# Kernel optimization log

Measured on AMD Instinct MI355X. Metric: run time of the kernel, lower is better.

Reference implementation:

```python
import jax, jax.numpy as jnp
import numpy as np

N = 100000      # nodes
E = 3200000     # edges (avg degree 32)
F_IN = 512
F_OUT = 256


def setup_inputs() -> dict:
    key = jax.random.key(0)
    k1, k2, k3, k4, k5, k6 = jax.random.split(key, 6)
    x = jax.random.normal(k1, (N, F_IN), dtype=jnp.float32)
    row = jax.random.randint(k2, (E,), 0, N)            # destination node of each edge
    col = jax.random.randint(k3, (E,), 0, N)            # source node of each edge
    edge_val = jax.random.uniform(k4, (E,), dtype=jnp.float32)  # normalized adj weights
    stdv = 1.0 / np.sqrt(F_OUT)                         # matches reset_parameters()
    weight = jax.random.uniform(k5, (F_IN, F_OUT), dtype=jnp.float32, minval=-stdv, maxval=stdv)
    bias = jax.random.uniform(k6, (F_OUT,), dtype=jnp.float32, minval=-stdv, maxval=stdv)
    return {"input": x, "weight": weight, "bias": bias, "edge_val": edge_val, "row": row, "col": col}


def reference(input, weight, bias, edge_val, row, col):
    # support = X @ W  (dense projection)
    support = input @ weight                             # [N, F_OUT]
    # SpMM: out[r] += a[r,c] * support[c] over COO edges (torch.spmm(adj, support))
    msgs = edge_val[:, None] * support[col]              # [E, F_OUT] gather + scale
    agg = jax.ops.segment_sum(msgs, row, num_segments=input.shape[0])  # scatter-add
    # np.around(..., decimals=3) applied row-wise in the original
    out = jnp.round(agg * 1000.0) / 1000.0
    return out + bias
```

## Files before the change

### kernel.cpp

```cpp
#include <hip/hip_runtime.h>

#define N_NODES 100000
#define N_EDGES 3200000
#define FIN 512
#define FOUT 256
#define GEMM_BM 64
#define GEMM_BK 32

#define NP 782
#define CAP_LDS 4608
#define SC_CHUNK 16384

typedef __attribute__((ext_vector_type(8))) short short8;
typedef __attribute__((ext_vector_type(4))) float f32x4;

__device__ __forceinline__ unsigned short f2bf(float f) {
    unsigned u = __float_as_uint(f);
    u += 0x7fffu + ((u >> 16) & 1u);
    return (unsigned short)(u >> 16);
}
__device__ __forceinline__ float bf2f(unsigned short h) {
    return __uint_as_float(((unsigned)h) << 16);
}

__global__ __launch_bounds__(256) void prep_weight(const float* __restrict__ W,
                                                   unsigned short* __restrict__ Wt) {
    int idx = blockIdx.x * 256 + threadIdx.x;
    if (idx < FIN * FOUT) {
        int k = idx >> 8;
        int n = idx & 255;
        Wt[(size_t)(k >> 5) * (FOUT * GEMM_BK) + n * GEMM_BK + (k & 31)] = f2bf(W[idx]);
    }
}

__global__ __launch_bounds__(256, 2)
void gemm_kernel(const float* __restrict__ X, const unsigned short* __restrict__ Wt,
                 unsigned short* __restrict__ support) {
    __shared__ unsigned short A_lds[GEMM_BM][40];
    __shared__ unsigned short B_lds[FOUT][40];

    const int t = threadIdx.x;
    const int lane = t & 63;
    const int wv = t >> 6;
    const int q = lane >> 4;
    const int lr = lane & 15;
    const int m0 = blockIdx.x * GEMM_BM;

    f32x4 acc[4][4];
#pragma unroll
    for (int i = 0; i < 4; i++)
#pragma unroll
        for (int j = 0; j < 4; j++) acc[i][j] = (f32x4)0.0f;

    const int arow = t >> 2;
    const int acol = (t & 3) * 8;
    const bool avalid = (m0 + arow) < N_NODES;
    const float* Xp = X + (size_t)(m0 + arow) * FIN + acol;

    for (int s = 0; s < FIN / GEMM_BK; ++s) {
        union { unsigned short us[8]; uint4 v; } pk;
        if (avalid) {
            float4 v0 = *(const float4*)(Xp + s * GEMM_BK);
            float4 v1 = *(const float4*)(Xp + s * GEMM_BK + 4);
            pk.us[0] = f2bf(v0.x); pk.us[1] = f2bf(v0.y);
            pk.us[2] = f2bf(v0.z); pk.us[3] = f2bf(v0.w);
            pk.us[4] = f2bf(v1.x); pk.us[5] = f2bf(v1.y);
            pk.us[6] = f2bf(v1.z); pk.us[7] = f2bf(v1.w);
        } else {
            pk.v = make_uint4(0, 0, 0, 0);
        }
        const uint4* bsrc = (const uint4*)(Wt + (size_t)s * (FOUT * GEMM_BK) + t * GEMM_BK);
        uint4 b0 = bsrc[0], b1 = bsrc[1], b2 = bsrc[2], b3 = bsrc[3];

        __syncthreads();
        *(uint4*)&A_lds[arow][acol] = pk.v;
        *(uint4*)&B_lds[t][0]  = b0;
        *(uint4*)&B_lds[t][8]  = b1;
        *(uint4*)&B_lds[t][16] = b2;
        *(uint4*)&B_lds[t][24] = b3;
        __syncthreads();

        short8 af[4], bfr[4];
#pragma unroll
        for (int i = 0; i < 4; i++) af[i] = *(const short8*)&A_lds[i * 16 + lr][q * 8];
#pragma unroll
        for (int j = 0; j < 4; j++) bfr[j] = *(const short8*)&B_lds[wv * 64 + j * 16 + lr][q * 8];
#pragma unroll
        for (int i = 0; i < 4; i++)
#pragma unroll
            for (int j = 0; j < 4; j++)
                acc[i][j] = __builtin_amdgcn_mfma_f32_16x16x32_bf16(af[i], bfr[j], acc[i][j], 0, 0, 0);
    }

#pragma unroll
    for (int i = 0; i < 4; i++) {
#pragma unroll
        for (int r = 0; r < 4; r++) {
            int gm = m0 + i * 16 + q * 4 + r;
            if (gm < N_NODES) {
#pragma unroll
                for (int j = 0; j < 4; j++)
                    support[(size_t)gm * FOUT + wv * 64 + j * 16 + lr] = f2bf(acc[i][j][r]);
            }
        }
    }
}

__global__ __launch_bounds__(256) void part_hist(const int* __restrict__ row,
                                                 unsigned* __restrict__ pcnt) {
    __shared__ unsigned bins[NP];
    for (int i = threadIdx.x; i < NP; i += 256) bins[i] = 0;
    __syncthreads();
    const int e0 = blockIdx.x * 8192;
#pragma unroll
    for (int j = 0; j < 32; ++j) {
        int e = e0 + j * 256 + threadIdx.x;
        if (e < N_EDGES) atomicAdd(&bins[((unsigned)row[e]) >> 7], 1u);
    }
    __syncthreads();
    for (int i = threadIdx.x; i < NP; i += 256)
        if (bins[i]) atomicAdd(&pcnt[i], bins[i]);
}

__global__ __launch_bounds__(1024) void part_scan(const unsigned* __restrict__ pcnt,
                                                  unsigned* __restrict__ base,
                                                  unsigned* __restrict__ cursor,
                                                  unsigned* __restrict__ row_ptr) {
    __shared__ unsigned s[1024];
    const int t = threadIdx.x;
    unsigned v = (t < NP) ? pcnt[t] : 0u;
    s[t] = v;
    __syncthreads();
#pragma unroll
    for (int off = 1; off < 1024; off <<= 1) {
        unsigned tv = (t >= off) ? s[t - off] : 0u;
        __syncthreads();
        s[t] += tv;
        __syncthreads();
    }
    if (t < NP) {
        unsigned b = s[t] - v;
        base[t] = b;
        cursor[t] = b;
    }
    if (t == 0) {
        base[NP] = N_EDGES;
        row_ptr[N_NODES] = N_EDGES;
    }
}

__global__ __launch_bounds__(256) void part_scatter(const int* __restrict__ row,
                                                    const int* __restrict__ col,
                                                    const float* __restrict__ val,
                                                    unsigned* __restrict__ cursor,
                                                    uint2* __restrict__ part) {
    __shared__ unsigned bins[NP];
    __shared__ unsigned gb[NP];
    for (int i = threadIdx.x; i < NP; i += 256) bins[i] = 0;
    __syncthreads();
    const int e0 = blockIdx.x * SC_CHUNK;
#pragma unroll 4
    for (int j = 0; j < SC_CHUNK / 256; ++j) {
        int e = e0 + j * 256 + threadIdx.x;
        if (e < N_EDGES) atomicAdd(&bins[((unsigned)row[e]) >> 7], 1u);
    }
    __syncthreads();
    for (int i = threadIdx.x; i < NP; i += 256) {
        unsigned c = bins[i];
        gb[i] = c ? atomicAdd(&cursor[i], c) : 0u;
        bins[i] = 0;
    }
    __syncthreads();
#pragma unroll 4
    for (int j = 0; j < SC_CHUNK / 256; ++j) {
        int e = e0 + j * 256 + threadIdx.x;
        if (e < N_EDGES) {
            unsigned r = (unsigned)row[e];
            unsigned p = r >> 7;
            unsigned l = atomicAdd(&bins[p], 1u);
            part[gb[p] + l] = make_uint2(((unsigned)col[e]) | ((r & 127u) << 17),
                                         __float_as_uint(val[e]));
        }
    }
}

__global__ __launch_bounds__(256) void part_finalize(const unsigned* __restrict__ base,
                                                     uint2* __restrict__ part,
                                                     unsigned* __restrict__ row_ptr) {
    __shared__ uint2 recs[CAP_LDS];
    __shared__ unsigned ncnt[128], nsc[128], ccur[128];
    const int p = blockIdx.x;
    const int t = threadIdx.x;
    const unsigned b = base[p];
    unsigned cnt = base[p + 1] - b;
    if (cnt > CAP_LDS) cnt = CAP_LDS;
    if (t < 128) ncnt[t] = 0;
    __syncthreads();
    for (unsigned i = t; i < cnt; i += 256) {
        uint2 r = part[b + i];
        recs[i] = r;
        atomicAdd(&ncnt[r.x >> 17], 1u);
    }
    __syncthreads();
    if (t < 128) nsc[t] = ncnt[t];
    __syncthreads();
#pragma unroll
    for (int off = 1; off < 128; off <<= 1) {
        unsigned tv = (t < 128 && t >= off) ? nsc[t - off] : 0u;
        __syncthreads();
        if (t < 128) nsc[t] += tv;
        __syncthreads();
    }
    if (t < 128) {
        unsigned ex = nsc[t] - ncnt[t];
        ccur[t] = ex;
        int node = p * 128 + t;
        if (node < N_NODES) row_ptr[node] = b + ex;
    }
    __syncthreads();
    for (unsigned i = t; i < cnt; i += 256) {
        uint2 r = recs[i];
        unsigned pos = atomicAdd(&ccur[r.x >> 17], 1u);
        part[b + pos] = make_uint2(r.x & 0x1FFFFu, r.y);
    }
}

__global__ __launch_bounds__(256)
void spmm_kernel(const unsigned* __restrict__ row_ptr, const uint2* __restrict__ sorted,
                 const unsigned short* __restrict__ support, const float* __restrict__ bias,
                 float* __restrict__ out) {
    const int lane = threadIdx.x & 63;
    const int n = blockIdx.x * 4 + (threadIdx.x >> 6);
    const unsigned start = row_ptr[n];
    const unsigned end = row_ptr[n + 1];
    const int fo = lane * 4;
    float a0 = 0.f, a1 = 0.f, a2 = 0.f, a3 = 0.f;

    unsigned i = start;
    for (; i + 4 <= end; i += 4) {
        uint2 e0 = sorted[i], e1 = sorted[i + 1], e2 = sorted[i + 2], e3 = sorted[i + 3];
        ushort4 s0 = *(const ushort4*)(support + (size_t)e0.x * FOUT + fo);
        ushort4 s1 = *(const ushort4*)(support + (size_t)e1.x * FOUT + fo);
        ushort4 s2 = *(const ushort4*)(support + (size_t)e2.x * FOUT + fo);
        ushort4 s3 = *(const ushort4*)(support + (size_t)e3.x * FOUT + fo);
        float v0 = __uint_as_float(e0.y), v1 = __uint_as_float(e1.y);
        float v2 = __uint_as_float(e2.y), v3 = __uint_as_float(e3.y);
        a0 += v0 * bf2f(s0.x); a1 += v0 * bf2f(s0.y); a2 += v0 * bf2f(s0.z); a3 += v0 * bf2f(s0.w);
        a0 += v1 * bf2f(s1.x); a1 += v1 * bf2f(s1.y); a2 += v1 * bf2f(s1.z); a3 += v1 * bf2f(s1.w);
        a0 += v2 * bf2f(s2.x); a1 += v2 * bf2f(s2.y); a2 += v2 * bf2f(s2.z); a3 += v2 * bf2f(s2.w);
        a0 += v3 * bf2f(s3.x); a1 += v3 * bf2f(s3.y); a2 += v3 * bf2f(s3.z); a3 += v3 * bf2f(s3.w);
    }
    for (; i < end; ++i) {
        uint2 e = sorted[i];
        ushort4 s = *(const ushort4*)(support + (size_t)e.x * FOUT + fo);
        float v = __uint_as_float(e.y);
        a0 += v * bf2f(s.x); a1 += v * bf2f(s.y); a2 += v * bf2f(s.z); a3 += v * bf2f(s.w);
    }

    float4 bv = *(const float4*)(bias + fo);
    float4 r;
    r.x = rintf(a0 * 1000.f) * 0.001f + bv.x;
    r.y = rintf(a1 * 1000.f) * 0.001f + bv.y;
    r.z = rintf(a2 * 1000.f) * 0.001f + bv.z;
    r.w = rintf(a3 * 1000.f) * 0.001f + bv.w;
    *(float4*)(out + (size_t)n * FOUT + fo) = r;
}

extern "C" void kernel_launch(void* const* d_in, const int* in_sizes, int n_in,
                              void* d_out, int out_size, void* d_ws, size_t ws_size,
                              hipStream_t stream) {
    (void)in_sizes; (void)n_in; (void)out_size; (void)ws_size;
    const float* X    = (const float*)d_in[0];
    const float* W    = (const float*)d_in[1];
    const float* bias = (const float*)d_in[2];
    const float* eval = (const float*)d_in[3];
    const int*   row  = (const int*)d_in[4];
    const int*   col  = (const int*)d_in[5];
    float* out = (float*)d_out;

    char* p = (char*)d_ws;
    auto take = [&](size_t bytes) {
        char* r = p;
        p += (bytes + 511) & ~(size_t)511;
        return r;
    };
    unsigned short* support = (unsigned short*)take((size_t)N_NODES * FOUT * 2);
    unsigned short* Wt      = (unsigned short*)take((size_t)FIN * FOUT * 2);
    unsigned*       pcnt    = (unsigned*)take((size_t)NP * 4);
    unsigned*       base    = (unsigned*)take((size_t)(NP + 1) * 4);
    unsigned*       cursor  = (unsigned*)take((size_t)NP * 4);
    unsigned*       row_ptr = (unsigned*)take((size_t)(N_NODES + 1) * 4);
    uint2*          part    = (uint2*)take((size_t)N_EDGES * 8);

    hipMemsetAsync(pcnt, 0, (size_t)NP * 4, stream);
    prep_weight<<<(FIN * FOUT) / 256, 256, 0, stream>>>(W, Wt);
    gemm_kernel<<<(N_NODES + GEMM_BM - 1) / GEMM_BM, 256, 0, stream>>>(X, Wt, support);
    part_hist<<<(N_EDGES + 8191) / 8192, 256, 0, stream>>>(row, pcnt);
    part_scan<<<1, 1024, 0, stream>>>(pcnt, base, cursor, row_ptr);
    part_scatter<<<(N_EDGES + SC_CHUNK - 1) / SC_CHUNK, 256, 0, stream>>>(row, col, eval, cursor, part);
    part_finalize<<<NP, 256, 0, stream>>>(base, part, row_ptr);
    spmm_kernel<<<N_NODES / 4, 256, 0, stream>>>(row_ptr, part, support, bias, out);
}
```

Measured before the change: 738.8 us.

## Enlarge GEMM tile to 128 rows with 8 waves; pipeline SpMM edge loads

The GEMM block grows to 128 rows with 512 threads arranged as a 2x4 wave grid, so each weight tile loaded into LDS is reused across twice as many rows. fp32-to-bf16 packing now uses the HIP bf16 intrinsics. The SpMM kernel makes the row bounds wave-uniform with readfirstlane and processes edges in batches of 8, prefetching the next batch's edge records while the current batch's support rows are gathered. This raises memory-level parallelism in the gather, at the cost of more registers and lower occupancy in both kernels.

```diff
diff --git a/kernel.cpp b/kernel.cpp
--- a/kernel.cpp
+++ b/kernel.cpp
@@ -1,10 +1,11 @@
 #include <hip/hip_runtime.h>
+#include <hip/hip_bf16.h>
 
 #define N_NODES 100000
 #define N_EDGES 3200000
 #define FIN 512
 #define FOUT 256
-#define GEMM_BM 64
+#define GEMM_BM 128
 #define GEMM_BK 32
 
 #define NP 782
@@ -33,7 +34,7 @@
     }
 }
 
-__global__ __launch_bounds__(256, 2)
+__global__ __launch_bounds__(512, 4)
 void gemm_kernel(const float* __restrict__ X, const unsigned short* __restrict__ Wt,
                  unsigned short* __restrict__ support) {
     __shared__ unsigned short A_lds[GEMM_BM][40];
@@ -41,7 +42,9 @@
 
     const int t = threadIdx.x;
     const int lane = t & 63;
-    const int wv = t >> 6;
+    const int w = t >> 6;
+    const int wm = w >> 2;
+    const int wn = w & 3;
     const int q = lane >> 4;
     const int lr = lane & 15;
     const int m0 = blockIdx.x * GEMM_BM;
@@ -57,34 +60,35 @@
     const bool avalid = (m0 + arow) < N_NODES;
     const float* Xp = X + (size_t)(m0 + arow) * FIN + acol;
 
+    const int brow = t >> 1;
+    const int bcol = (t & 1) * 16;
+
     for (int s = 0; s < FIN / GEMM_BK; ++s) {
-        union { unsigned short us[8]; uint4 v; } pk;
+        union { __hip_bfloat162 h[4]; uint4 v; } pk;
         if (avalid) {
             float4 v0 = *(const float4*)(Xp + s * GEMM_BK);
             float4 v1 = *(const float4*)(Xp + s * GEMM_BK + 4);
-            pk.us[0] = f2bf(v0.x); pk.us[1] = f2bf(v0.y);
-            pk.us[2] = f2bf(v0.z); pk.us[3] = f2bf(v0.w);
-            pk.us[4] = f2bf(v1.x); pk.us[5] = f2bf(v1.y);
-            pk.us[6] = f2bf(v1.z); pk.us[7] = f2bf(v1.w);
+            pk.h[0] = __float22bfloat162_rn(make_float2(v0.x, v0.y));
+            pk.h[1] = __float22bfloat162_rn(make_float2(v0.z, v0.w));
+            pk.h[2] = __float22bfloat162_rn(make_float2(v1.x, v1.y));
+            pk.h[3] = __float22bfloat162_rn(make_float2(v1.z, v1.w));
         } else {
             pk.v = make_uint4(0, 0, 0, 0);
         }
-        const uint4* bsrc = (const uint4*)(Wt + (size_t)s * (FOUT * GEMM_BK) + t * GEMM_BK);
-        uint4 b0 = bsrc[0], b1 = bsrc[1], b2 = bsrc[2], b3 = bsrc[3];
+        const uint4* bsrc = (const uint4*)(Wt + (size_t)s * (FOUT * GEMM_BK) + brow * GEMM_BK + bcol);
+        uint4 b0 = bsrc[0], b1 = bsrc[1];
 
         __syncthreads();
         *(uint4*)&A_lds[arow][acol] = pk.v;
-        *(uint4*)&B_lds[t][0]  = b0;
-        *(uint4*)&B_lds[t][8]  = b1;
-        *(uint4*)&B_lds[t][16] = b2;
-        *(uint4*)&B_lds[t][24] = b3;
+        *(uint4*)&B_lds[brow][bcol] = b0;
+        *(uint4*)&B_lds[brow][bcol + 8] = b1;
         __syncthreads();
 
         short8 af[4], bfr[4];
 #pragma unroll
-        for (int i = 0; i < 4; i++) af[i] = *(const short8*)&A_lds[i * 16 + lr][q * 8];
-#pragma unroll
-        for (int j = 0; j < 4; j++) bfr[j] = *(const short8*)&B_lds[wv * 64 + j * 16 + lr][q * 8];
+        for (int i = 0; i < 4; i++) af[i] = *(const short8*)&A_lds[wm * 64 + i * 16 + lr][q * 8];
+#pragma unroll
+        for (int j = 0; j < 4; j++) bfr[j] = *(const short8*)&B_lds[wn * 64 + j * 16 + lr][q * 8];
 #pragma unroll
         for (int i = 0; i < 4; i++)
 #pragma unroll
@@ -96,11 +100,11 @@
     for (int i = 0; i < 4; i++) {
 #pragma unroll
         for (int r = 0; r < 4; r++) {
-            int gm = m0 + i * 16 + q * 4 + r;
+            int gm = m0 + wm * 64 + i * 16 + q * 4 + r;
             if (gm < N_NODES) {
 #pragma unroll
                 for (int j = 0; j < 4; j++)
-                    support[(size_t)gm * FOUT + wv * 64 + j * 16 + lr] = f2bf(acc[i][j][r]);
+                    support[(size_t)gm * FOUT + wn * 64 + j * 16 + lr] = f2bf(acc[i][j][r]);
             }
         }
     }
@@ -231,30 +235,51 @@
                  float* __restrict__ out) {
     const int lane = threadIdx.x & 63;
     const int n = blockIdx.x * 4 + (threadIdx.x >> 6);
-    const unsigned start = row_ptr[n];
-    const unsigned end = row_ptr[n + 1];
+    const unsigned start = __builtin_amdgcn_readfirstlane(row_ptr[n]);
+    const unsigned end   = __builtin_amdgcn_readfirstlane(row_ptr[n + 1]);
     const int fo = lane * 4;
+    const unsigned short* sp = support + fo;
     float a0 = 0.f, a1 = 0.f, a2 = 0.f, a3 = 0.f;
 
     unsigned i = start;
-    for (; i + 4 <= end; i += 4) {
-        uint2 e0 = sorted[i], e1 = sorted[i + 1], e2 = sorted[i + 2], e3 = sorted[i + 3];
-        ushort4 s0 = *(const ushort4*)(support + (size_t)e0.x * FOUT + fo);
-        ushort4 s1 = *(const ushort4*)(support + (size_t)e1.x * FOUT + fo);
-        ushort4 s2 = *(const ushort4*)(support + (size_t)e2.x * FOUT + fo);
-        ushort4 s3 = *(const ushort4*)(support + (size_t)e3.x * FOUT + fo);
-        float v0 = __uint_as_float(e0.y), v1 = __uint_as_float(e1.y);
-        float v2 = __uint_as_float(e2.y), v3 = __uint_as_float(e3.y);
-        a0 += v0 * bf2f(s0.x); a1 += v0 * bf2f(s0.y); a2 += v0 * bf2f(s0.z); a3 += v0 * bf2f(s0.w);
-        a0 += v1 * bf2f(s1.x); a1 += v1 * bf2f(s1.y); a2 += v1 * bf2f(s1.z); a3 += v1 * bf2f(s1.w);
-        a0 += v2 * bf2f(s2.x); a1 += v2 * bf2f(s2.y); a2 += v2 * bf2f(s2.z); a3 += v2 * bf2f(s2.w);
-        a0 += v3 * bf2f(s3.x); a1 += v3 * bf2f(s3.y); a2 += v3 * bf2f(s3.z); a3 += v3 * bf2f(s3.w);
+    const unsigned nfull = (end - start) >> 3;
+    if (nfull) {
+        uint2 e[8];
+#pragma unroll
+        for (int j = 0; j < 8; ++j) e[j] = sorted[i + j];
+        for (unsigned bt = 1; bt < nfull; ++bt) {
+            ushort4 s[8];
+#pragma unroll
+            for (int j = 0; j < 8; ++j) s[j] = *(const ushort4*)(sp + (size_t)e[j].x * FOUT);
+            uint2 en[8];
+#pragma unroll
+            for (int j = 0; j < 8; ++j) en[j] = sorted[i + 8 + j];
+#pragma unroll
+            for (int j = 0; j < 8; ++j) {
+                float v = __uint_as_float(e[j].y);
+                a0 += v * bf2f(s[j].x); a1 += v * bf2f(s[j].y);
+                a2 += v * bf2f(s[j].z); a3 += v * bf2f(s[j].w);
+            }
+#pragma unroll
+            for (int j = 0; j < 8; ++j) e[j] = en[j];
+            i += 8;
+        }
+        ushort4 s[8];
+#pragma unroll
+        for (int j = 0; j < 8; ++j) s[j] = *(const ushort4*)(sp + (size_t)e[j].x * FOUT);
+#pragma unroll
+        for (int j = 0; j < 8; ++j) {
+            float v = __uint_as_float(e[j].y);
+            a0 += v * bf2f(s[j].x); a1 += v * bf2f(s[j].y);
+            a2 += v * bf2f(s[j].z); a3 += v * bf2f(s[j].w);
+        }
+        i += 8;
     }
     for (; i < end; ++i) {
         uint2 e = sorted[i];
-        ushort4 s = *(const ushort4*)(support + (size_t)e.x * FOUT + fo);
         float v = __uint_as_float(e.y);
-        a0 += v * bf2f(s.x); a1 += v * bf2f(s.y); a2 += v * bf2f(s.z); a3 += v * bf2f(s.w);
+        ushort4 s0 = *(const ushort4*)(sp + (size_t)e.x * FOUT);
+        a0 += v * bf2f(s0.x); a1 += v * bf2f(s0.y); a2 += v * bf2f(s0.z); a3 += v * bf2f(s0.w);
     }
 
     float4 bv = *(const float4*)(bias + fo);
@@ -294,7 +319,7 @@
 
     hipMemsetAsync(pcnt, 0, (size_t)NP * 4, stream);
     prep_weight<<<(FIN * FOUT) / 256, 256, 0, stream>>>(W, Wt);
-    gemm_kernel<<<(N_NODES + GEMM_BM - 1) / GEMM_BM, 256, 0, stream>>>(X, Wt, support);
+    gemm_kernel<<<(N_NODES + GEMM_BM - 1) / GEMM_BM, 512, 0, stream>>>(X, Wt, support);
     part_hist<<<(N_EDGES + 8191) / 8192, 256, 0, stream>>>(row, pcnt);
     part_scan<<<1, 1024, 0, stream>>>(pcnt, base, cursor, row_ptr);
     part_scatter<<<(N_EDGES + SC_CHUNK - 1) / SC_CHUNK, 256, 0, stream>>>(row, col, eval, cursor, part);
```

Result: faster. 719.0 us (-2.7%).
